# Performance work log

Measured on AMD Instinct MI355X. Metric: run time of the kernel, lower is better.

Reference implementation:

```python
import jax, jax.numpy as jnp
import numpy as np

ALPHA = 0.2  # LeakyReLU negative slope


def setup_inputs() -> dict:
    key = jax.random.key(0)
    k1, k2, k3 = jax.random.split(key, 3)
    B, N, F_in, F_out = 8, 2048, 256, 128
    h = jax.random.normal(k1, (B, N, F_in), dtype=jnp.float32)
    # nn.Linear(in, out, bias=False) weight applied as h @ W (stored [in, out])
    W = jax.random.normal(k2, (F_in, F_out), dtype=jnp.float32) * (1.0 / np.sqrt(F_in))
    # attention vector a: Linear(2*F_out, 1) -> vector of length 2*F_out
    a = jax.random.normal(k3, (2 * F_out,), dtype=jnp.float32) * (1.0 / np.sqrt(2 * F_out))
    return {"h": h, "W": W, "a": a}


def reference(h, W, a):
    # Wh: [B, N, F_out]
    Wh = jnp.einsum("bni,io->bno", h, W)
    F_out = W.shape[1]
    a1, a2 = a[:F_out], a[F_out:]
    # a(cat(Wh_i, Wh_j)) == Wh_i @ a1 + Wh_j @ a2 -- identical math, no O(N^2*2F) concat
    s1 = Wh @ a1  # [B, N] (source/row term)
    s2 = Wh @ a2  # [B, N] (target/col term)
    e = jax.nn.leaky_relu(s1[:, :, None] + s2[:, None, :], negative_slope=ALPHA)  # [B, N, N]
    attention = jax.nn.softmax(e, axis=-1)
    # dropout on attention is identity in eval mode (deterministic baseline)
    h_prime = jnp.einsum("bij,bjf->bif", attention, Wh)  # [B, N, F_out]
    return jax.nn.elu(h_prime)
```

## Files before the change

kernel.cpp:

```cpp
#include <hip/hip_runtime.h>
#include <math.h>
#include <stdint.h>

#define B_    8
#define N_    2048
#define FIN   256
#define FO    128
#define ALPHA 0.2f
#define NCHUNK 32
#define CHUNK  64

typedef __attribute__((ext_vector_type(8))) __bf16 bf16x8;
typedef __attribute__((ext_vector_type(8))) short short8_t;
typedef __attribute__((ext_vector_type(4))) short short4_t;
typedef __attribute__((ext_vector_type(4))) float f32x4;

static const size_t OFF_WH    = 0;
static const size_t OFF_S1P   = OFF_WH    + (size_t)B_*N_*FO;
static const size_t OFF_S2P   = OFF_S1P   + (size_t)4*B_*N_;
static const size_t OFF_SSORT = OFF_S2P   + (size_t)4*B_*N_;
static const size_t OFF_SORD  = OFF_SSORT + (size_t)B_*N_;
static const size_t OFF_E2P   = OFF_SORD  + (size_t)B_*N_;
static const size_t OFF_E2N   = OFF_E2P   + (size_t)B_*N_;
static const size_t OFF_DPN   = OFF_E2N   + (size_t)B_*N_;
static const size_t OFF_KCUT  = OFF_DPN   + (size_t)2*B_*N_;
static const size_t OFF_SPN   = OFF_KCUT  + (size_t)B_*N_;

__device__ __forceinline__ unsigned short bf16_rne(float x) {
    unsigned u = __float_as_uint(x);
    unsigned r = (u + 0x7FFFu + ((u >> 16) & 1u)) >> 16;
    return (unsigned short)r;
}

__global__ __launch_bounds__(512) void k1_gemm(const float* __restrict__ h,
                                               const float* __restrict__ W,
                                               const float* __restrict__ a,
                                               float* __restrict__ Wh,
                                               float* __restrict__ s1p,
                                               float* __restrict__ s2p) {
    __shared__ short hS_hi[64][40], hS_lo[64][40];
    __shared__ short wS_hi[128][40], wS_lo[128][40];

    const int tid  = threadIdx.x;
    const int lane = tid & 63, wv = tid >> 6;
    const int mh = wv & 1, ng = wv >> 1;
    const int l15 = lane & 15, l4 = lane >> 4;
    const int row0 = blockIdx.x * 64;

    const int h_r = tid >> 3, h_kq = (tid & 7) * 4;
    const int w_c = tid & 127, w_kb = (tid >> 7) * 8;

    f32x4 acc[2][2];
#pragma unroll
    for (int i = 0; i < 2; ++i)
#pragma unroll
        for (int j = 0; j < 2; ++j) acc[i][j] = (f32x4){0.f, 0.f, 0.f, 0.f};

    float4 hv = *(const float4*)&h[(size_t)(row0 + h_r) * FIN + h_kq];
    float wf[8];
#pragma unroll
    for (int s = 0; s < 8; ++s) wf[s] = W[(size_t)(w_kb + s) * FO + w_c];

    for (int k0 = 0; k0 < FIN; k0 += 32) {
        {
            float hf[4] = {hv.x, hv.y, hv.z, hv.w};
            short4_t hhi, hlo;
#pragma unroll
            for (int s = 0; s < 4; ++s) {
                unsigned short hb = bf16_rne(hf[s]);
                float hbf = __uint_as_float((unsigned)hb << 16);
                hhi[s] = (short)hb;
                hlo[s] = (short)bf16_rne(hf[s] - hbf);
            }
            *(short4_t*)&hS_hi[h_r][h_kq] = hhi;
            *(short4_t*)&hS_lo[h_r][h_kq] = hlo;

            short8_t whi, wlo;
#pragma unroll
            for (int s = 0; s < 8; ++s) {
                unsigned short wb = bf16_rne(wf[s]);
                float wbf = __uint_as_float((unsigned)wb << 16);
                whi[s] = (short)wb;
                wlo[s] = (short)bf16_rne(wf[s] - wbf);
            }
            *(short8_t*)&wS_hi[w_c][w_kb] = whi;
            *(short8_t*)&wS_lo[w_c][w_kb] = wlo;
        }
        __syncthreads();

        if (k0 + 32 < FIN) {
            hv = *(const float4*)&h[(size_t)(row0 + h_r) * FIN + k0 + 32 + h_kq];
#pragma unroll
            for (int s = 0; s < 8; ++s)
                wf[s] = W[(size_t)(k0 + 32 + w_kb + s) * FO + w_c];
        }

        bf16x8 a_hi[2], a_lo[2], b_hi[2], b_lo[2];
#pragma unroll
        for (int i = 0; i < 2; ++i) {
            int r = (mh * 2 + i) * 16 + l15;
            a_hi[i] = __builtin_bit_cast(bf16x8, *(short8_t*)&hS_hi[r][l4 * 8]);
            a_lo[i] = __builtin_bit_cast(bf16x8, *(short8_t*)&hS_lo[r][l4 * 8]);
        }
#pragma unroll
        for (int j = 0; j < 2; ++j) {
            int c = (ng * 2 + j) * 16 + l15;
            b_hi[j] = __builtin_bit_cast(bf16x8, *(short8_t*)&wS_hi[c][l4 * 8]);
            b_lo[j] = __builtin_bit_cast(bf16x8, *(short8_t*)&wS_lo[c][l4 * 8]);
        }
#pragma unroll
        for (int i = 0; i < 2; ++i)
#pragma unroll
            for (int j = 0; j < 2; ++j) {
                acc[i][j] = __builtin_amdgcn_mfma_f32_16x16x32_bf16(a_hi[i], b_hi[j], acc[i][j], 0, 0, 0);
                acc[i][j] = __builtin_amdgcn_mfma_f32_16x16x32_bf16(a_hi[i], b_lo[j], acc[i][j], 0, 0, 0);
                acc[i][j] = __builtin_amdgcn_mfma_f32_16x16x32_bf16(a_lo[i], b_hi[j], acc[i][j], 0, 0, 0);
            }
        __syncthreads();
    }

#pragma unroll
    for (int i = 0; i < 2; ++i)
#pragma unroll
        for (int j = 0; j < 2; ++j) {
            int colg = (ng * 2 + j) * 16 + l15;
#pragma unroll
            for (int reg = 0; reg < 4; ++reg) {
                int rowg = row0 + (mh * 2 + i) * 16 + l4 * 4 + reg;
                Wh[(size_t)rowg * FO + colg] = acc[i][j][reg];
            }
        }

    float a1v[2], a2v[2];
#pragma unroll
    for (int j = 0; j < 2; ++j) {
        int c = (ng * 2 + j) * 16 + l15;
        a1v[j] = a[c];
        a2v[j] = a[FO + c];
    }
#pragma unroll
    for (int i = 0; i < 2; ++i) {
        float p1[4], p2[4];
#pragma unroll
        for (int reg = 0; reg < 4; ++reg) {
            p1[reg] = acc[i][0][reg] * a1v[0] + acc[i][1][reg] * a1v[1];
            p2[reg] = acc[i][0][reg] * a2v[0] + acc[i][1][reg] * a2v[1];
        }
#pragma unroll
        for (int m = 1; m < 16; m <<= 1) {
#pragma unroll
            for (int reg = 0; reg < 4; ++reg) {
                p1[reg] += __shfl_xor(p1[reg], m);
                p2[reg] += __shfl_xor(p2[reg], m);
            }
        }
        if (l15 == 0) {
#pragma unroll
            for (int reg = 0; reg < 4; ++reg) {
                int rowg = row0 + (mh * 2 + i) * 16 + l4 * 4 + reg;
                s1p[(size_t)ng * (B_ * N_) + rowg] = p1[reg];
                s2p[(size_t)ng * (B_ * N_) + rowg] = p2[reg];
            }
        }
    }
}

__global__ __launch_bounds__(512) void k2a_rank(const float* __restrict__ s2p,
                                                float* __restrict__ ssort,
                                                int* __restrict__ sord,
                                                float* __restrict__ e2p,
                                                float* __restrict__ e2n) {
    __shared__ uint64_t keys[N_];
    __shared__ int part[512];
    const int b = blockIdx.x >> 5, c = blockIdx.x & 31;
    const int tid = threadIdx.x;
    const size_t SZ = (size_t)B_ * N_;

    for (int t = tid; t < N_; t += 512) {
        size_t ix = (size_t)b * N_ + t;
        float s2v = s2p[ix] + s2p[SZ + ix] + s2p[2 * SZ + ix] + s2p[3 * SZ + ix];
        unsigned u = __float_as_uint(s2v);
        u = (u & 0x80000000u) ? ~u : (u | 0x80000000u);
        keys[t] = ((uint64_t)u << 16) | (unsigned)t;
    }
    __syncthreads();

    const int le = tid & 63;
    const int e  = c * 64 + le;
    const int q  = tid >> 6;
    const uint64_t myk = keys[e];
    const uint64_t* kp = keys + q * 256;
    int cnt = 0;
#pragma unroll 8
    for (int kk = 0; kk < 256; ++kk) cnt += (int)(kp[kk] > myk);
    part[tid] = cnt;
    __syncthreads();

    if (tid < 64) {
        int rank = 0;
#pragma unroll
        for (int g = 0; g < 8; ++g) rank += part[tid + 64 * g];
        int ee = c * 64 + tid;
        size_t ix = (size_t)b * N_ + ee;
        float v = s2p[ix] + s2p[SZ + ix] + s2p[2 * SZ + ix] + s2p[3 * SZ + ix];
        ssort[b * N_ + rank] = v;
        sord[b * N_ + rank]  = ee;
        e2p[b * N_ + rank] = expf(v);
        e2n[b * N_ + rank] = expf(ALPHA * v);
    }
}

__global__ __launch_bounds__(512) void kx_scan(const float* __restrict__ Wh,
                                               const int* __restrict__ sord,
                                               const float* __restrict__ e2p,
                                               const float* __restrict__ e2n,
                                               const float* __restrict__ ssort,
                                               const float* __restrict__ s1p,
                                               float2* __restrict__ SPN,
                                               float2* __restrict__ DPN,
                                               int* __restrict__ kcut) {
    __shared__ float2 qt[4][FO];
    __shared__ float sv[N_];
    __shared__ float2 wsum[8];
    const int tid = threadIdx.x;
    const int bid = blockIdx.x;
    const size_t SZ = (size_t)B_ * N_;

    if (bid < 256) {
        const int b = bid >> 5, ch = bid & 31;
        const int f = tid & 127, q = tid >> 7;
        const size_t base = (size_t)b * N_;
        const int ks = ch * CHUNK + q * 16;

        int ords[16]; float wp[16], wn[16], xv[16];
#pragma unroll
        for (int j = 0; j < 16; ++j) ords[j] = sord[base + ks + j];
#pragma unroll
        for (int j = 0; j < 16; ++j) { wp[j] = e2p[base + ks + j]; wn[j] = e2n[base + ks + j]; }
#pragma unroll
        for (int j = 0; j < 16; ++j) xv[j] = Wh[(base + ords[j]) * FO + f];

        float2 s[16];
        float ap = 0.f, an = 0.f;
#pragma unroll
        for (int j = 0; j < 16; ++j) {
            ap += wp[j] * xv[j];
            an += wn[j] * xv[j];
            s[j] = make_float2(ap, an);
        }
        qt[q][f] = make_float2(ap, an);
        __syncthreads();

        float op = 0.f, on = 0.f;
#pragma unroll
        for (int q2 = 0; q2 < 3; ++q2)
            if (q2 < q) { op += qt[q2][f].x; on += qt[q2][f].y; }

#pragma unroll
        for (int j = 0; j < 16; ++j)
            SPN[(base + ks + j) * FO + f] = make_float2(s[j].x + op, s[j].y + on);
    } else {
        const int b = bid - 256;
        const size_t base = (size_t)b * N_;

        float v[4], pv[4], nv[4], lp[4], ln[4];
        *(float4*)&v[0]  = *(const float4*)&ssort[base + tid * 4];
        *(float4*)&pv[0] = *(const float4*)&e2p[base + tid * 4];
        *(float4*)&nv[0] = *(const float4*)&e2n[base + tid * 4];
        float ap = 0.f, an = 0.f;
#pragma unroll
        for (int j = 0; j < 4; ++j) {
            sv[tid * 4 + j] = v[j];
            ap += pv[j]; lp[j] = ap;
            an += nv[j]; ln[j] = an;
        }

        float ip = ap, in2 = an;
        const int lane = tid & 63;
#pragma unroll
        for (int off = 1; off < 64; off <<= 1) {
            float tpv = __shfl_up(ip, off);
            float tnv = __shfl_up(in2, off);
            if (lane >= off) { ip += tpv; in2 += tnv; }
        }
        if (lane == 63) wsum[tid >> 6] = make_float2(ip, in2);
        __syncthreads();

        float basP = ip - ap, basN = in2 - an;
        const int w = tid >> 6;
#pragma unroll
        for (int w2 = 0; w2 < 7; ++w2)
            if (w2 < w) { basP += wsum[w2].x; basN += wsum[w2].y; }
#pragma unroll
        for (int j = 0; j < 4; ++j)
            DPN[base + tid * 4 + j] = make_float2(lp[j] + basP, ln[j] + basN);

        float tgt[4];
        int lo[4], hi[4];
#pragma unroll
        for (int r = 0; r < 4; ++r) {
            size_t row = base + tid + 512 * r;
            tgt[r] = -(s1p[row] + s1p[SZ + row] + s1p[2 * SZ + row] + s1p[3 * SZ + row]);
            lo[r] = 0; hi[r] = N_;
        }
#pragma unroll
        for (int step = 0; step < 11; ++step) {
#pragma unroll
            for (int r = 0; r < 4; ++r) {
                int mid = (lo[r] + hi[r]) >> 1;
                bool live = lo[r] < hi[r];
                float pv2 = sv[mid & (N_ - 1)];
                bool cc = live && (pv2 >= tgt[r]);
                lo[r] = cc ? mid + 1 : lo[r];
                hi[r] = (live && !cc) ? mid : hi[r];
            }
        }
#pragma unroll
        for (int r = 0; r < 4; ++r) kcut[base + tid + 512 * r] = lo[r];
    }
}

__global__ __launch_bounds__(512) void k4_final(const float* __restrict__ s1p,
                                                const int* __restrict__ kcut,
                                                const float2* __restrict__ DPN,
                                                const float2* __restrict__ SPN,
                                                float* __restrict__ out) {
    __shared__ float2 ct[NCHUNK][FO];
    __shared__ float2 qTot[4][FO];
    __shared__ float sntN_lds[FO];
    __shared__ float2 s1e_lds[32];
    __shared__ float2 dpn_lds[32];
    __shared__ int    k_lds[32];

    const int bid = blockIdx.x;
    const int b   = bid >> 6;
    const int r0  = (bid & 63) * 32;
    const int tid = threadIdx.x;
    const int f = tid & 127, rr = tid >> 7;
    const size_t base = (size_t)b * N_;
    const size_t SZ = (size_t)B_ * N_;

    for (int idx = tid; idx < NCHUNK * FO; idx += 512) {
        int c = idx >> 7, ff = idx & 127;
        ct[c][ff] = SPN[(base + c * CHUNK + CHUNK - 1) * FO + ff];
    }
    if (tid < 32) {
        int row = r0 + tid;
        int k = kcut[base + row];
        k_lds[tid] = k;
        size_t rix = base + row;
        float s1v = s1p[rix] + s1p[SZ + rix] + s1p[2 * SZ + rix] + s1p[3 * SZ + rix];
        s1e_lds[tid] = make_float2(expf(s1v), expf(ALPHA * s1v));
        dpn_lds[tid] = (k > 0) ? DPN[base + k - 1] : make_float2(0.f, 0.f);
    }
    __syncthreads();

    float rp = 0.f, rn = 0.f;
    for (int c = rr * 8; c < rr * 8 + 8; ++c) {
        float2 t = ct[c][f];
        ct[c][f] = make_float2(rp, rn);
        rp += t.x; rn += t.y;
    }
    qTot[rr][f] = make_float2(rp, rn);
    __syncthreads();
    float addP = 0.f, addN = 0.f;
#pragma unroll
    for (int q2 = 0; q2 < 3; ++q2)
        if (q2 < rr) { addP += qTot[q2][f].x; addN += qTot[q2][f].y; }
    if (rr > 0) {
        for (int c = rr * 8; c < rr * 8 + 8; ++c) {
            float2 t = ct[c][f];
            ct[c][f] = make_float2(t.x + addP, t.y + addN);
        }
    }
    if (tid < FO)
        sntN_lds[tid] = qTot[0][tid].y + qTot[1][tid].y + qTot[2][tid].y + qTot[3][tid].y;
    __syncthreads();

    const float dnt = DPN[base + N_ - 1].y;
    const float sntN = sntN_lds[f];

#pragma unroll 2
    for (int it = 0; it < 8; ++it) {
        const int lr   = it * 4 + rr;
        const int row  = r0 + lr;
        const float2 e1 = s1e_lds[lr];
        const float2 d  = dpn_lds[lr];
        const int k = k_lds[lr];

        float sp = 0.f, sn = 0.f;
        if (k > 0) {
            const int km1 = k - 1;
            const int c32 = km1 >> 6;
            float2 o  = ct[c32][f];
            float2 sl = SPN[(base + km1) * FO + f];
            sp = o.x + sl.x;
            sn = o.y + sl.y;
        }
        const float den = e1.x * d.x + e1.y * (dnt - d.y);
        const float num = e1.x * sp + e1.y * (sntN - sn);
        const float o = num / den;
        out[((size_t)b * N_ + row) * FO + f] = (o > 0.f) ? o : (expf(o) - 1.f);
    }
}

extern "C" void kernel_launch(void* const* d_in, const int* in_sizes, int n_in,
                              void* d_out, int out_size, void* d_ws, size_t ws_size,
                              hipStream_t stream) {
    const float* h = (const float*)d_in[0];
    const float* W = (const float*)d_in[1];
    const float* a = (const float*)d_in[2];
    float* out = (float*)d_out;
    float* ws = (float*)d_ws;

    float*  Wh    = ws + OFF_WH;
    float*  s1p   = ws + OFF_S1P;
    float*  s2p   = ws + OFF_S2P;
    float*  ssort = ws + OFF_SSORT;
    int*    sord  = (int*)(ws + OFF_SORD);
    float*  e2p   = ws + OFF_E2P;
    float*  e2n   = ws + OFF_E2N;
    float2* DPN   = (float2*)(ws + OFF_DPN);
    int*    kcut  = (int*)(ws + OFF_KCUT);
    float2* SPN   = (float2*)(ws + OFF_SPN);

    k1_gemm<<<dim3(B_ * N_ / 64), dim3(512), 0, stream>>>(h, W, a, Wh, s1p, s2p);
    k2a_rank<<<dim3(B_ * 32), dim3(512), 0, stream>>>(s2p, ssort, sord, e2p, e2n);
    kx_scan<<<dim3(264), dim3(512), 0, stream>>>(Wh, sord, e2p, e2n, ssort, s1p,
                                                 SPN, DPN, kcut);
    k4_final<<<dim3(512), dim3(512), 0, stream>>>(s1p, kcut, DPN, SPN, out);
}
```

Measured before the change: 45.35 us.

## Store only every fourth prefix row and reconstruct the remainder in final kernel

The scan kernel now writes only one in four rows of the per-feature prefix-sum array SPN, which cuts its global write traffic to a quarter. The final kernel rebuilds the needed prefix value from the nearest stored row plus up to three weighted Wh rows, gathered through the sort order and the e2p/e2n weights. All loads are hoisted into a batched prefetch loop ahead of the compute loop. This adds gathers and register pressure in the final kernel, and the fallback logic at chunk boundaries is subtle.

After: 61.07 us. 34.7% more time.

```diff
diff --git a/kernel.cpp b/kernel.cpp
--- a/kernel.cpp
+++ b/kernel.cpp
@@ -257,7 +257,7 @@
             if (q2 < q) { op += qt[q2][f].x; on += qt[q2][f].y; }
 
 #pragma unroll
-        for (int j = 0; j < 16; ++j)
+        for (int j = 3; j < 16; j += 4)
             SPN[(base + ks + j) * FO + f] = make_float2(s[j].x + op, s[j].y + on);
     } else {
         const int b = bid - 256;
@@ -324,6 +324,10 @@
                                                 const int* __restrict__ kcut,
                                                 const float2* __restrict__ DPN,
                                                 const float2* __restrict__ SPN,
+                                                const float* __restrict__ Wh,
+                                                const int* __restrict__ sord,
+                                                const float* __restrict__ e2p,
+                                                const float* __restrict__ e2n,
                                                 float* __restrict__ out) {
     __shared__ float2 ct[NCHUNK][FO];
     __shared__ float2 qTot[4][FO];
@@ -380,22 +384,49 @@
     const float dnt = DPN[base + N_ - 1].y;
     const float sntN = sntN_lds[f];
 
-#pragma unroll 2
+    float2 sl[8], ov[8];
+    float tx[8][3], twp[8][3], twn[8][3];
+    int kv[8];
+#pragma unroll
     for (int it = 0; it < 8; ++it) {
-        const int lr   = it * 4 + rr;
-        const int row  = r0 + lr;
+        const int lr = it * 4 + rr;
+        const int k = k_lds[lr];
+        kv[it] = k;
+        const int km1 = (k > 0) ? (k - 1) : 0;
+        const int c32 = km1 >> 6;
+        const int rem = (k > 0) ? ((km1 + 1) & 3) : 0;
+        const int pbase = km1 - rem;
+        const bool useSPN = (k > 0) && (rem == 0 || (pbase >= 0 && (pbase >> 6) == c32));
+        const int spnIdx = (rem == 0) ? km1 : (useSPN ? pbase : km1);
+        sl[it] = useSPN ? SPN[(base + spnIdx) * FO + f] : make_float2(0.f, 0.f);
+        ov[it] = (k > 0) ? ct[c32][f] : make_float2(0.f, 0.f);
+#pragma unroll
+        for (int t = 0; t < 3; ++t) {
+            const bool act = (k > 0) && (t < rem);
+            int j = pbase + 1 + t;
+            j = act ? j : km1;
+            const int ord = sord[base + j];
+            twp[it][t] = act ? e2p[base + j] : 0.f;
+            twn[it][t] = act ? e2n[base + j] : 0.f;
+            tx[it][t]  = Wh[(base + ord) * FO + f];
+        }
+    }
+#pragma unroll
+    for (int it = 0; it < 8; ++it) {
+        const int lr  = it * 4 + rr;
+        const int row = r0 + lr;
         const float2 e1 = s1e_lds[lr];
         const float2 d  = dpn_lds[lr];
-        const int k = k_lds[lr];
 
         float sp = 0.f, sn = 0.f;
-        if (k > 0) {
-            const int km1 = k - 1;
-            const int c32 = km1 >> 6;
-            float2 o  = ct[c32][f];
-            float2 sl = SPN[(base + km1) * FO + f];
-            sp = o.x + sl.x;
-            sn = o.y + sl.y;
+        if (kv[it] > 0) {
+            sp = ov[it].x + sl[it].x;
+            sn = ov[it].y + sl[it].y;
+#pragma unroll
+            for (int t = 0; t < 3; ++t) {
+                sp += twp[it][t] * tx[it][t];
+                sn += twn[it][t] * tx[it][t];
+            }
         }
         const float den = e1.x * d.x + e1.y * (dnt - d.y);
         const float num = e1.x * sp + e1.y * (sntN - sn);
@@ -428,5 +459,6 @@
     k2a_rank<<<dim3(B_ * 32), dim3(512), 0, stream>>>(s2p, ssort, sord, e2p, e2n);
     kx_scan<<<dim3(264), dim3(512), 0, stream>>>(Wh, sord, e2p, e2n, ssort, s1p,
                                                  SPN, DPN, kcut);
-    k4_final<<<dim3(512), dim3(512), 0, stream>>>(s1p, kcut, DPN, SPN, out);
-}
+    k4_final<<<dim3(512), dim3(512), 0, stream>>>(s1p, kcut, DPN, SPN,
+                                                  Wh, sord, e2p, e2n, out);
+}
```
